# Optimization experiments

Hardware: AMD Instinct MI355X
Metric: run time of the kernel (lower is better)

Reference implementation:

```python
import jax, jax.numpy as jnp
import numpy as np

B, S, D = 1, 2048, 1024
H, HD = 16, 64            # heads, head_dim = D // H
TEN, ED, K = 32, 128, 8   # experts, expert_dim, top_k
DS = 2048                 # shared expert dim
THETA = 10000.0
EPS = 1e-6
RSF = 2.5                 # routed_scaling_factor


def setup_inputs() -> dict:
    key = jax.random.key(0)
    ks = jax.random.split(key, 12)
    s = 0.02
    return {
        "x_input": jax.random.normal(ks[0], (B, S, D), jnp.float32),
        "indices": jax.random.randint(ks[1], (B * S, K), 0, TEN, dtype=jnp.int32),
        "values": jax.random.normal(ks[2], (B * S, K), jnp.float32),
        "w_attn": jax.random.normal(ks[3], (D, 3 * D), jnp.float32) * s,
        "w_attn_o": jax.random.normal(ks[4], (D, D), jnp.float32) * s,
        "attn_norm_w": jnp.ones((D,), jnp.float32),
        "ffn_norm_w": jnp.ones((D,), jnp.float32),
        "ffn_experts": jax.random.normal(ks[5], (3, TEN, D, ED), jnp.float32) * s,
        "keys_w": jax.random.normal(ks[6], (D, TEN), jnp.float32) * s,
        "w_up": jax.random.normal(ks[7], (D, 2 * DS), jnp.float32) * s,
        "w_down": jax.random.normal(ks[8], (DS, D), jnp.float32) * s,
    }


def rmsnorm(x, w):
    return x * jax.lax.rsqrt(jnp.mean(x * x, -1, keepdims=True) + EPS) * w


def l2norm(x):
    # F.normalize(x, dim=-1, eps=EPS)
    n = jnp.sqrt(jnp.sum(x * x, -1, keepdims=True))
    return x / jnp.maximum(n, EPS)


def rope(x):
    # x: [B, H, S, HD]
    t = jnp.arange(x.shape[2], dtype=jnp.float32)
    inv = (1.0 / THETA) ** (jnp.arange(0, HD, 2, dtype=jnp.float32) / HD)
    f = jnp.outer(t, inv)[None, None]  # [1,1,S,HD//2]
    cos, sin = jnp.cos(f), jnp.sin(f)
    x1, x2 = jnp.split(x, 2, -1)
    return jnp.concatenate([x1 * cos + x2 * sin, -x1 * sin + x2 * cos], -1)


def reference(x_input, indices, values, w_attn, w_attn_o, attn_norm_w,
              ffn_norm_w, ffn_experts, keys_w, w_up, w_down):
    # ---- attention block ----
    x = rmsnorm(x_input, attn_norm_w)
    qkv = x @ w_attn  # [B,S,3D]
    xq, xk, xv = jnp.split(qkv, 3, -1)
    to_heads = lambda t: t.reshape(B, S, H, HD).transpose(0, 2, 1, 3)  # b h s a
    xq, xk, xv = to_heads(xq), to_heads(xk), to_heads(xv)
    xq, xk = l2norm(xq), l2norm(xk)  # qk_norm
    xq, xk = rope(xq), rope(xk)
    scores = jnp.einsum('bhqd,bhkd->bhqk', xq, xk) / jnp.sqrt(jnp.float32(HD))
    causal = jnp.tril(jnp.ones((S, S), bool))
    scores = jnp.where(causal, scores, jnp.finfo(scores.dtype).min)
    probs = jax.nn.softmax(scores, -1)
    x_attn = jnp.einsum('bhqk,bhkd->bhqd', probs, xv)
    x_attn = x_attn.transpose(0, 2, 1, 3).reshape(B, S, D)
    x_attn_o = x_attn @ w_attn_o
    x_ffn_input = x_attn_o + x_input

    # ---- router ----
    x_ffn = rmsnorm(x_ffn_input, ffn_norm_w)
    xf = x_ffn.reshape(B * S, D)
    logits = xf @ keys_w  # [T, TEN]
    token_values = jnp.take_along_axis(logits, indices, -1)  # [T, K]
    gates = jax.nn.sigmoid(values + token_values) * RSF

    # ---- grouped-GEMM expert dispatch (dense equivalent: combine is linear in score) ----
    T = B * S
    w_route = jnp.zeros((T, TEN), xf.dtype).at[jnp.arange(T)[:, None], indices].add(gates)
    g = jnp.einsum('td,edh->teh', xf, ffn_experts[0])
    u = jnp.einsum('td,edh->teh', xf, ffn_experts[1])
    h = jax.nn.silu(g) * u * w_route[:, :, None]
    y = jnp.einsum('teh,edh->td', h, ffn_experts[2]).reshape(B, S, D)

    # ---- shared expert (SwiGLU FFN) ----
    x1, x2 = jnp.split(x_ffn @ w_up, 2, -1)
    y_shared = (jax.nn.silu(x1) * x2) @ w_down
    y = y + y_shared
    return y + x_ffn_input
```

## Files before the change

### kernel.cpp

```cpp
#include <hip/hip_runtime.h>
#include <math.h>

#define TOKENS 2048
#define DIM 1024
#define NHEADS 16
#define HEADDIM 64
#define NEXP 32
#define EDIM 128
#define TOPK 8
#define DSHARED 2048
#define RSF_ 2.5f
#define EPS_ 1e-6f

using bf8  = __attribute__((ext_vector_type(8))) short;
using f32x4 = __attribute__((ext_vector_type(4))) float;

__device__ __forceinline__ short f2bf(float f) {
    unsigned u = __float_as_uint(f);
    unsigned r = (u + 0x7fffu + ((u >> 16) & 1u)) >> 16;
    return (short)r;
}
__device__ __forceinline__ float bf2f(short s) {
    return __uint_as_float(((unsigned)(unsigned short)s) << 16);
}

__device__ __forceinline__ void async16(const short* g, const short* l) {
    __builtin_amdgcn_global_load_lds(
        (const __attribute__((address_space(1))) void*)(unsigned long long)g,
        (__attribute__((address_space(3))) void*)(unsigned)(unsigned long long)l,
        16, 0, 0);
}

__global__ __launch_bounds__(256) void rmsnorm_kernel(const float* __restrict__ x,
                                                      const float* __restrict__ w,
                                                      short* __restrict__ out) {
    int row = blockIdx.x;
    const float* xr = x + (long long)row * DIM;
    int t = threadIdx.x;
    float4 xv = ((const float4*)xr)[t];
    float ss = xv.x*xv.x + xv.y*xv.y + xv.z*xv.z + xv.w*xv.w;
    #pragma unroll
    for (int off = 32; off; off >>= 1) ss += __shfl_down(ss, off);
    __shared__ float warps[4];
    if ((t & 63) == 0) warps[t >> 6] = ss;
    __syncthreads();
    float tot = warps[0] + warps[1] + warps[2] + warps[3];
    float scale = rsqrtf(tot / (float)DIM + EPS_);
    float4 wv = ((const float4*)w)[t];
    short4 o;
    o.x = f2bf(xv.x * scale * wv.x);
    o.y = f2bf(xv.y * scale * wv.y);
    o.z = f2bf(xv.z * scale * wv.z);
    o.w = f2bf(xv.w * scale * wv.w);
    ((short4*)(out + (long long)row * DIM))[t] = o;
}

__global__ __launch_bounds__(256) void tconv(const float* __restrict__ in, long long sin,
                                             short* __restrict__ out, long long sout,
                                             int K, int N) {
    in  += (long long)blockIdx.z * sin;
    out += (long long)blockIdx.z * sout;
    __shared__ float t[32][33];
    int n0 = blockIdx.x * 32, k0 = blockIdx.y * 32;
    int tx = threadIdx.x & 31, ty = threadIdx.x >> 5;
    #pragma unroll
    for (int r = ty; r < 32; r += 8)
        t[r][tx] = in[(long long)(k0 + r) * N + n0 + tx];
    __syncthreads();
    #pragma unroll
    for (int r = ty; r < 32; r += 8)
        out[(long long)(n0 + r) * K + k0 + tx] = f2bf(t[tx][r]);
}

__global__ void w2conv(const float* __restrict__ in, short* __restrict__ out) {
    long long i = (long long)blockIdx.x * 256 + threadIdx.x;
    int e = (int)(i >> 17);
    int d = (int)(i >> 7) & 1023;
    int h = (int)(i & 127);
    out[(long long)d * (NEXP * EDIM) + e * EDIM + h] = f2bf(in[i]);
}

template<int MODE>
__global__ __launch_bounds__(256) void gemm_bf16(const short* __restrict__ A, int lda, long long sA,
                                                 const short* __restrict__ Bt, int ldb, long long sBt,
                                                 void* __restrict__ Cv, int ldc, long long sC,
                                                 int M, int N, int K) {
    int koff = 0, Ksub = K;
    if (MODE >= 3) {
        Ksub = K / gridDim.z;
        koff = blockIdx.z * Ksub;
    } else {
        A  += (long long)blockIdx.z * sA;
        Bt += (long long)blockIdx.z * sBt;
    }
    float* Cf = (float*)Cv;
    short* Cs = (short*)Cv;
    Cf += (long long)blockIdx.z * sC;
    Cs += (long long)blockIdx.z * sC;
    const int m0 = blockIdx.y * 128, n0 = blockIdx.x * 128;
    __shared__ short As[128 * 64];
    __shared__ short Bs[128 * 64];
    const int tid = threadIdx.x, lane = tid & 63, w = tid >> 6;
    const int wm = (w >> 1) * 64, wn = (w & 1) * 64;
    const int drow = lane >> 3;
    const int dcol = ((lane & 7) ^ drow) * 8;
    const short* ag = A + (long long)(m0 + w * 32 + drow) * lda + koff + dcol;
    const short* bg = Bt + (long long)(n0 + w * 32 + drow) * ldb + koff + dcol;
    const short* lA = As + w * 32 * 64;
    const short* lB = Bs + w * 32 * 64;
    f32x4 acc[4][4];
    #pragma unroll
    for (int i = 0; i < 4; ++i)
        #pragma unroll
        for (int j = 0; j < 4; ++j) { f32x4 z = {0.f, 0.f, 0.f, 0.f}; acc[i][j] = z; }
    const int ra = lane & 15, quad = lane >> 4;
    const int fs0 = ((quad + 0) ^ (ra & 7)) * 8;
    const int fs1 = ((quad + 4) ^ (ra & 7)) * 8;
    for (int k0 = 0; k0 < Ksub; k0 += 64) {
        #pragma unroll
        for (int c = 0; c < 4; ++c) {
            async16(ag + (long long)(c * 8) * lda + k0, lA + c * 512);
            async16(bg + (long long)(c * 8) * ldb + k0, lB + c * 512);
        }
        __syncthreads();
        #pragma unroll
        for (int h = 0; h < 2; ++h) {
            const int fs = h ? fs1 : fs0;
            bf8 af[4], bfv[4];
            #pragma unroll
            for (int i = 0; i < 4; ++i) af[i]  = *(const bf8*)(As + (wm + i * 16 + ra) * 64 + fs);
            #pragma unroll
            for (int j = 0; j < 4; ++j) bfv[j] = *(const bf8*)(Bs + (wn + j * 16 + ra) * 64 + fs);
            #pragma unroll
            for (int i = 0; i < 4; ++i)
                #pragma unroll
                for (int j = 0; j < 4; ++j)
                    acc[i][j] = __builtin_amdgcn_mfma_f32_16x16x32_bf16(af[i], bfv[j], acc[i][j], 0, 0, 0);
        }
        __syncthreads();
    }
    const int cr = quad * 4, cc = ra;
    #pragma unroll
    for (int i = 0; i < 4; ++i) {
        #pragma unroll
        for (int r = 0; r < 4; ++r) {
            int row = m0 + wm + i * 16 + cr + r;
            long long base = (long long)row * ldc + n0 + wn + cc;
            #pragma unroll
            for (int j = 0; j < 4; ++j) {
                float v = acc[i][j][r];
                if (MODE == 0 || MODE == 3) Cf[base + j * 16] = v;
                if (MODE == 2) Cs[base + j * 16] = f2bf(v);
                if (MODE == 4) Cf[base + j * 16] = Cf[base + j * 16] + v;
            }
        }
    }
}

__global__ void combine4(const float* __restrict__ slices, const float* __restrict__ add,
                         float* __restrict__ dst) {
    long long i = (long long)blockIdx.x * 256 + threadIdx.x;
    const long long S4 = (long long)TOKENS * DIM / 4;
    float4 s = ((const float4*)add)[i];
    #pragma unroll
    for (int c = 0; c < 4; ++c) {
        float4 p = ((const float4*)slices)[c * S4 + i];
        s.x += p.x; s.y += p.y; s.z += p.z; s.w += p.w;
    }
    ((float4*)dst)[i] = s;
}

__global__ __launch_bounds__(256) void qkv_post(const short* __restrict__ qkv,
                                                short* __restrict__ q,
                                                short* __restrict__ k) {
    int lane = threadIdx.x & 63;
    int sh = blockIdx.x * 4 + (threadIdx.x >> 6);
    int s = sh >> 4;
    int h = sh & 15;
    const short* base = qkv + (long long)s * 3 * DIM;
    float qv = bf2f(base[h * HEADDIM + lane]);
    float kv = bf2f(base[DIM + h * HEADDIM + lane]);
    float qs = qv * qv, ks = kv * kv;
    #pragma unroll
    for (int off = 32; off; off >>= 1) {
        qs += __shfl_xor(qs, off);
        ks += __shfl_xor(ks, off);
    }
    qv /= fmaxf(sqrtf(qs), EPS_);
    kv /= fmaxf(sqrtf(ks), EPS_);
    int i = lane & 31;
    float f = (float)s * powf(10000.0f, -(float)i / 32.0f);
    float c = cosf(f), sn = sinf(f);
    float qo = __shfl_xor(qv, 32);
    float ko = __shfl_xor(kv, 32);
    float sgn = (lane < 32) ? sn : -sn;
    float qr = qv * c + qo * sgn;
    float kr = kv * c + ko * sgn;
    long long o = ((long long)h * TOKENS + s) * HEADDIM + lane;
    q[o] = f2bf(qr);
    k[o] = f2bf(kr);
}

__global__ __launch_bounds__(256) void vtrans(const short* __restrict__ qkv,
                                              short* __restrict__ vt) {
    int h = blockIdx.z;
    int s0 = blockIdx.x * 32, d0 = blockIdx.y * 32;
    __shared__ short t[32][34];
    int tx = threadIdx.x & 31, ty = threadIdx.x >> 5;
    #pragma unroll
    for (int r = ty; r < 32; r += 8)
        t[r][tx] = qkv[(long long)(s0 + r) * (3 * DIM) + 2 * DIM + h * HEADDIM + d0 + tx];
    __syncthreads();
    #pragma unroll
    for (int r = ty; r < 32; r += 8)
        vt[((long long)h * HEADDIM + d0 + r) * TOKENS + s0 + tx] = t[tx][r];
}

#define PLD 68
__global__ __launch_bounds__(256) void attn_kernel(const short* __restrict__ q,
                                                   const short* __restrict__ k,
                                                   const short* __restrict__ vt,
                                                   float* __restrict__ Oacc,
                                                   float* __restrict__ lacc) {
    const int w = threadIdx.x >> 6, lane = threadIdx.x & 63;
    const int col = lane & 15, quad = lane >> 4;
    const int head = blockIdx.x / 80;
    const int t = blockIdx.x % 80;
    int qb, ch;
    if (t < 8)       { qb = t;                ch = 0; }
    else if (t < 24) { qb = 8 + (t - 8) / 2;  ch = (t - 8) % 2; }
    else if (t < 48) { qb = 16 + (t - 24) / 3; ch = (t - 24) % 3; }
    else             { qb = 24 + (t - 48) / 4; ch = (t - 48) % 4; }
    const int nch = qb / 8 + 1;
    const int ntk = qb + 1;
    const int per = (ntk + nch - 1) / nch;
    const int t0 = ch * per;
    const int t1 = (t0 + per < ntk) ? t0 + per : ntk;
    const int qbase = qb * 64 + w * 16;
    __shared__ short Ks[64 * 64];
    __shared__ short Vs[64 * 64];
    __shared__ short Ps[4 * 16 * PLD];
    short* Pw = Ps + w * 16 * PLD;
    const short* kh = k + (long long)head * TOKENS * HEADDIM;
    const short* vh = vt + (long long)head * HEADDIM * TOKENS;
    const int r8 = lane >> 3;
    const int sw = ((lane & 7) ^ r8) * 8;
    bf8 qf[2];
    #pragma unroll
    for (int ks = 0; ks < 2; ++ks)
        qf[ks] = *(const bf8*)(q + ((long long)head * TOKENS + qbase + col) * HEADDIM + ks * 32 + quad * 8);
    const int fo0 = (((0 * 4) + quad) ^ (col & 7)) * 8;
    const int fo1 = (((1 * 4) + quad) ^ (col & 7)) * 8;
    f32x4 o_[4];
    float l_[4];
    #pragma unroll
    for (int n = 0; n < 4; ++n) { f32x4 z = {0.f, 0.f, 0.f, 0.f}; o_[n] = z; }
    #pragma unroll
    for (int r = 0; r < 4; ++r) l_[r] = 0.f;
    for (int kt = t0; kt < t1; ++kt) {
        const int j0 = kt * 64;
        #pragma unroll
        for (int c = 0; c < 2; ++c) {
            int row = w * 16 + c * 8 + r8;
            async16(kh + (long long)(j0 + row) * HEADDIM + sw, Ks + (w * 16 + c * 8) * 64 + lane * 8);
            async16(vh + (long long)row * TOKENS + j0 + sw, Vs + (w * 16 + c * 8) * 64 + lane * 8);
        }
        __syncthreads();
        f32x4 sacc[4];
        #pragma unroll
        for (int n = 0; n < 4; ++n) { f32x4 z = {0.f, 0.f, 0.f, 0.f}; sacc[n] = z; }
        #pragma unroll
        for (int ks = 0; ks < 2; ++ks) {
            const int fo = ks ? fo1 : fo0;
            #pragma unroll
            for (int nt = 0; nt < 4; ++nt) {
                bf8 kf = *(const bf8*)(Ks + (nt * 16 + col) * 64 + fo);
                sacc[nt] = __builtin_amdgcn_mfma_f32_16x16x32_bf16(qf[ks], kf, sacc[nt], 0, 0, 0);
            }
        }
        const bool diag = (j0 + 64 > qbase);
        #pragma unroll
        for (int nt = 0; nt < 4; ++nt)
            #pragma unroll
            for (int r = 0; r < 4; ++r) {
                float p = __expf(sacc[nt][r] * 0.125f);
                if (diag && (j0 + nt * 16 + col > qbase + quad * 4 + r)) p = 0.f;
                l_[r] += p;
                Pw[(quad * 4 + r) * PLD + nt * 16 + col] = f2bf(p);
            }
        #pragma unroll
        for (int ks = 0; ks < 2; ++ks) {
            bf8 pf = *(const bf8*)(Pw + col * PLD + ks * 32 + quad * 8);
            const int fo = ks ? fo1 : fo0;
            #pragma unroll
            for (int nt = 0; nt < 4; ++nt) {
                bf8 vf = *(const bf8*)(Vs + (nt * 16 + col) * 64 + fo);
                o_[nt] = __builtin_amdgcn_mfma_f32_16x16x32_bf16(pf, vf, o_[nt], 0, 0, 0);
            }
        }
        __syncthreads();
    }
    float* Oc = Oacc + (long long)ch * (TOKENS * DIM);
    #pragma unroll
    for (int r = 0; r < 4; ++r) {
        int row = qbase + quad * 4 + r;
        float* op = Oc + (long long)row * DIM + head * HEADDIM;
        #pragma unroll
        for (int nt = 0; nt < 4; ++nt)
            op[nt * 16 + col] = o_[nt][r];
        float l = l_[r];
        #pragma unroll
        for (int off = 1; off < 16; off <<= 1) l += __shfl_xor(l, off);
        if (col == 0) lacc[ch * (TOKENS * NHEADS) + row * NHEADS + head] = l;
    }
}

__global__ void attn_norm(const float* __restrict__ Oacc, const float* __restrict__ lacc,
                          short* __restrict__ xo) {
    long long i = (long long)blockIdx.x * 256 + threadIdx.x;
    int row = (int)(i >> 10), col = (int)(i & 1023);
    int nch = (row >> 9) + 1;
    int head = col >> 6;
    float so = 0.f, sl = 0.f;
    for (int c = 0; c < nch; ++c) {
        so += Oacc[(long long)c * (TOKENS * DIM) + i];
        sl += lacc[c * (TOKENS * NHEADS) + row * NHEADS + head];
    }
    xo[i] = f2bf(so / sl);
}

__global__ __launch_bounds__(256) void router_kernel(const short* __restrict__ xf,
                                                     const float* __restrict__ keys_w,
                                                     const int* __restrict__ idx,
                                                     const float* __restrict__ vals,
                                                     float* __restrict__ w_route) {
    int t = blockIdx.x;
    int tid = threadIdx.x;
    int e = tid & 31, c = tid >> 5;
    const short* xr = xf + (long long)t * DIM;
    float p = 0.f;
    for (int j = 0; j < 128; ++j)
        p += bf2f(xr[c * 128 + j]) * keys_w[(c * 128 + j) * NEXP + e];
    __shared__ float part[8][32];
    part[c][e] = p;
    __syncthreads();
    if (tid < NEXP) {
        float lg = 0.f;
        #pragma unroll
        for (int cc = 0; cc < 8; ++cc) lg += part[cc][tid];
        part[0][tid] = lg;
    }
    __syncthreads();
    __shared__ float gate_s[TOPK];
    __shared__ int idx_s[TOPK];
    if (tid < TOPK) {
        int ii = idx[t * TOPK + tid];
        float g = vals[t * TOPK + tid] + part[0][ii];
        gate_s[tid] = (1.0f / (1.0f + __expf(-g))) * RSF_;
        idx_s[tid] = ii;
    }
    __syncthreads();
    if (tid < NEXP) {
        float wr = 0.f;
        #pragma unroll
        for (int kk = 0; kk < TOPK; ++kk)
            if (idx_s[kk] == tid) wr += gate_s[kk];
        w_route[(long long)t * NEXP + tid] = wr;
    }
}

__global__ void moe_act_kernel(const short* __restrict__ gu, const float* __restrict__ w_route,
                               short* __restrict__ hb) {
    long long i = (long long)blockIdx.x * 256 + threadIdx.x;
    int t = (int)(i >> 12);
    int e = (int)(i >> 7) & 31;
    int j = (int)(i & 127);
    float gv = bf2f(gu[(long long)t * (NEXP * 256) + e * 256 + j]);
    float uv = bf2f(gu[(long long)t * (NEXP * 256) + e * 256 + 128 + j]);
    float w = w_route[t * NEXP + e];
    float si = gv / (1.0f + __expf(-gv));
    hb[i] = f2bf(si * uv * w);
}

__global__ void swiglu_kernel(const short* __restrict__ up, short* __restrict__ hs) {
    long long i = (long long)blockIdx.x * 256 + threadIdx.x;
    int t = (int)(i >> 11), j = (int)(i & 2047);
    float x1 = bf2f(up[(long long)t * (2 * DSHARED) + j]);
    float x2 = bf2f(up[(long long)t * (2 * DSHARED) + DSHARED + j]);
    hs[i] = f2bf(x1 / (1.0f + __expf(-x1)) * x2);
}

extern "C" void kernel_launch(void* const* d_in, const int* in_sizes, int n_in,
                              void* d_out, int out_size, void* d_ws, size_t ws_size,
                              hipStream_t stream) {
    (void)in_sizes; (void)n_in; (void)out_size; (void)ws_size;
    const float* x_input     = (const float*)d_in[0];
    const int*   indices     = (const int*)d_in[1];
    const float* values      = (const float*)d_in[2];
    const float* w_attn      = (const float*)d_in[3];
    const float* w_attn_o    = (const float*)d_in[4];
    const float* attn_norm_w = (const float*)d_in[5];
    const float* ffn_norm_w  = (const float*)d_in[6];
    const float* ffn_experts = (const float*)d_in[7];
    const float* keys_w      = (const float*)d_in[8];
    const float* w_up        = (const float*)d_in[9];
    const float* w_down      = (const float*)d_in[10];
    float* out = (float*)d_out;
    float* ws  = (float*)d_ws;

    const long long M1 = 1024 * 1024;
    const long long SLICE = (long long)TOKENS * DIM;
    float* xffn    = ws + 0 * M1;
    short* xa_bf   = (short*)(ws + 4 * M1);
    short* xf_bf   = (short*)(ws + 4 * M1 + M1 / 2);
    short* xattn_bf= (short*)(ws + 5 * M1);
    float* w_route = ws + 5 * M1 + M1 / 2;
    short* qkv_bf  = (short*)(ws + 6 * M1);
    float* Oacc    = ws + 6 * M1;
    float* lacc    = ws + 14 * M1;
    short* qh_bf   = (short*)(ws + 15 * M1);
    short* kh_bf   = (short*)(ws + 15 * M1 + M1 / 2);
    short* vt_bf   = (short*)(ws + 16 * M1);
    short* wattn_t = (short*)(ws + 17 * M1);
    short* wattno_t= (short*)(ws + 18 * M1 + M1 / 2);
    float* oslice  = ws + 6 * M1;
    short* wgu     = (short*)(ws + 6 * M1);
    short* gu_bf   = (short*)(ws + 10 * M1);
    short* h_bf    = (short*)(ws + 18 * M1);
    short* w2t     = (short*)(ws + 22 * M1);
    float* yslice  = ws + 6 * M1;
    short* wupt    = (short*)(ws + 14 * M1);
    short* up_bf   = (short*)(ws + 16 * M1);
    short* hs_bf   = (short*)(ws + 20 * M1);
    short* wdownt  = (short*)(ws + 22 * M1);

    const long long EXP_STRIDE = (long long)NEXP * DIM * EDIM;

    tconv<<<dim3(3072 / 32, DIM / 32, 1), 256, 0, stream>>>(w_attn, 0, wattn_t, 0, DIM, 3 * DIM);
    rmsnorm_kernel<<<TOKENS, 256, 0, stream>>>(x_input, attn_norm_w, xa_bf);
    gemm_bf16<2><<<dim3(3072 / 128, TOKENS / 128, 1), 256, 0, stream>>>(
        xa_bf, DIM, 0, wattn_t, DIM, 0, qkv_bf, 3 * DIM, 0, TOKENS, 3 * DIM, DIM);
    qkv_post<<<(TOKENS * NHEADS) / 4, 256, 0, stream>>>(qkv_bf, qh_bf, kh_bf);
    vtrans<<<dim3(TOKENS / 32, HEADDIM / 32, NHEADS), 256, 0, stream>>>(qkv_bf, vt_bf);
    attn_kernel<<<NHEADS * 80, 256, 0, stream>>>(qh_bf, kh_bf, vt_bf, Oacc, lacc);
    attn_norm<<<(TOKENS * DIM) / 256, 256, 0, stream>>>(Oacc, lacc, xattn_bf);
    tconv<<<dim3(DIM / 32, DIM / 32, 1), 256, 0, stream>>>(w_attn_o, 0, wattno_t, 0, DIM, DIM);
    gemm_bf16<3><<<dim3(DIM / 128, TOKENS / 128, 4), 256, 0, stream>>>(
        xattn_bf, DIM, 0, wattno_t, DIM, 0, oslice, DIM, SLICE, TOKENS, DIM, DIM);
    combine4<<<(TOKENS * DIM) / 1024, 256, 0, stream>>>(oslice, x_input, xffn);

    rmsnorm_kernel<<<TOKENS, 256, 0, stream>>>(xffn, ffn_norm_w, xf_bf);
    router_kernel<<<TOKENS, 256, 0, stream>>>(xf_bf, keys_w, indices, values, w_route);
    tconv<<<dim3(EDIM / 32, DIM / 32, NEXP), 256, 0, stream>>>(
        ffn_experts, (long long)DIM * EDIM, wgu, 256 * 1024, DIM, EDIM);
    tconv<<<dim3(EDIM / 32, DIM / 32, NEXP), 256, 0, stream>>>(
        ffn_experts + EXP_STRIDE, (long long)DIM * EDIM, wgu + 128 * 1024, 256 * 1024, DIM, EDIM);
    gemm_bf16<2><<<dim3(2, TOKENS / 128, NEXP), 256, 0, stream>>>(
        xf_bf, DIM, 0, wgu, DIM, 256 * 1024, gu_bf, NEXP * 256, 256, TOKENS, 256, DIM);
    moe_act_kernel<<<(TOKENS * NEXP * EDIM) / 256, 256, 0, stream>>>(gu_bf, w_route, h_bf);
    w2conv<<<(NEXP * DIM * EDIM) / 256, 256, 0, stream>>>(ffn_experts + 2 * EXP_STRIDE, w2t);
    gemm_bf16<3><<<dim3(DIM / 128, TOKENS / 128, 4), 256, 0, stream>>>(
        h_bf, NEXP * EDIM, 0, w2t, NEXP * EDIM, 0, yslice, DIM, SLICE, TOKENS, DIM, NEXP * EDIM);

    tconv<<<dim3((2 * DSHARED) / 32, DIM / 32, 1), 256, 0, stream>>>(w_up, 0, wupt, 0, DIM, 2 * DSHARED);
    gemm_bf16<2><<<dim3((2 * DSHARED) / 128, TOKENS / 128, 1), 256, 0, stream>>>(
        xf_bf, DIM, 0, wupt, DIM, 0, up_bf, 2 * DSHARED, 0, TOKENS, 2 * DSHARED, DIM);
    swiglu_kernel<<<(TOKENS * DSHARED) / 256, 256, 0, stream>>>(up_bf, hs_bf);
    tconv<<<dim3(DIM / 32, DSHARED / 32, 1), 256, 0, stream>>>(w_down, 0, wdownt, 0, DSHARED, DIM);
    gemm_bf16<4><<<dim3(DIM / 128, TOKENS / 128, 4), 256, 0, stream>>>(
        hs_bf, DSHARED, 0, wdownt, DSHARED, 0, yslice, DIM, SLICE, TOKENS, DIM, DSHARED);

    combine4<<<(TOKENS * DIM) / 1024, 256, 0, stream>>>(yslice, xffn, out);
}
```

Measured before the change: 444.6 us.

## Fuse SwiGLU activations into gate/up GEMM epilogues and fuse residual with RMSNorm

Adds a gemm_act kernel that computes the gate and up projections together, using interleaved weight rows produced by new guconv/upconv transposes, and applies SiLU(g)*u (optionally scaled by the routing weight) in the epilogue. This removes the separate moe_act and swiglu passes and the bf16 intermediate gate/up tensors. It also merges combine4 with the second rmsnorm into one combine_rms kernel, and reorganizes workspace offsets. The risk is that the new GEMM uses 64-row tiles without double buffering, which may be less efficient than the existing gemm_bf16.

```diff
diff --git a/kernel.cpp b/kernel.cpp
--- a/kernel.cpp
+++ b/kernel.cpp
@@ -78,6 +78,45 @@
     int d = (int)(i >> 7) & 1023;
     int h = (int)(i & 127);
     out[(long long)d * (NEXP * EDIM) + e * EDIM + h] = f2bf(in[i]);
+}
+
+__global__ __launch_bounds__(256) void guconv(const float* __restrict__ ex,
+                                              short* __restrict__ wgu) {
+    int z = blockIdx.z;
+    int e = z & 31, hf = z >> 5;
+    const float* in = ex + (long long)hf * (NEXP * DIM * EDIM) + (long long)e * (DIM * EDIM);
+    short* outp = wgu + (long long)e * (256 * 1024);
+    __shared__ float t[32][33];
+    int n0 = blockIdx.x * 32, k0 = blockIdx.y * 32;
+    int tx = threadIdx.x & 31, ty = threadIdx.x >> 5;
+    #pragma unroll
+    for (int r = ty; r < 32; r += 8)
+        t[r][tx] = in[(long long)(k0 + r) * EDIM + n0 + tx];
+    __syncthreads();
+    #pragma unroll
+    for (int r = ty; r < 32; r += 8) {
+        int c = n0 + r;
+        int rr = ((c >> 4) << 5) + hf * 16 + (c & 15);
+        outp[(long long)rr * 1024 + k0 + tx] = f2bf(t[tx][r]);
+    }
+}
+
+__global__ __launch_bounds__(256) void upconv(const float* __restrict__ in,
+                                              short* __restrict__ outp) {
+    __shared__ float t[32][33];
+    int n0 = blockIdx.x * 32, k0 = blockIdx.y * 32;
+    int tx = threadIdx.x & 31, ty = threadIdx.x >> 5;
+    #pragma unroll
+    for (int r = ty; r < 32; r += 8)
+        t[r][tx] = in[(long long)(k0 + r) * (2 * DSHARED) + n0 + tx];
+    __syncthreads();
+    #pragma unroll
+    for (int r = ty; r < 32; r += 8) {
+        int n = n0 + r;
+        int hf = n >> 11, c2 = n & 2047;
+        int rr = ((c2 >> 7) << 8) + (((c2 & 127) >> 4) << 5) + hf * 16 + (c2 & 15);
+        outp[(long long)rr * 1024 + k0 + tx] = f2bf(t[tx][r]);
+    }
 }
 
 template<int MODE>
@@ -149,12 +188,75 @@
             #pragma unroll
             for (int j = 0; j < 4; ++j) {
                 float v = acc[i][j][r];
-                if (MODE == 0 || MODE == 3) Cf[base + j * 16] = v;
                 if (MODE == 2) Cs[base + j * 16] = f2bf(v);
+                if (MODE == 3) Cf[base + j * 16] = v;
                 if (MODE == 4) Cf[base + j * 16] = Cf[base + j * 16] + v;
             }
         }
     }
+}
+
+template<bool SCALED>
+__global__ __launch_bounds__(256) void gemm_act(const short* __restrict__ A, int lda,
+                                                const short* __restrict__ Bt, long long sBt,
+                                                short* __restrict__ Ct, int ldct,
+                                                const float* __restrict__ wr) {
+    const short* Bp = Bt + (long long)blockIdx.z * sBt + (long long)blockIdx.x * (256 * 1024);
+    const int cb = (blockIdx.z * gridDim.x + blockIdx.x) * 128;
+    const int m0 = blockIdx.y * 64;
+    __shared__ short As[64 * 64];
+    __shared__ short Bs[256 * 64];
+    const int tid = threadIdx.x, lane = tid & 63, w = tid >> 6;
+    const int wm = (w >> 1) * 32, wn = (w & 1) * 128;
+    const int drow = lane >> 3;
+    const int dcol = ((lane & 7) ^ drow) * 8;
+    const short* ag = A + (long long)(m0 + w * 16 + drow) * lda + dcol;
+    const short* bg = Bp + (long long)(w * 64 + drow) * 1024 + dcol;
+    const short* lA = As + w * 16 * 64;
+    const short* lB = Bs + w * 64 * 64;
+    f32x4 acc[2][8];
+    #pragma unroll
+    for (int i = 0; i < 2; ++i)
+        #pragma unroll
+        for (int j = 0; j < 8; ++j) { f32x4 z = {0.f, 0.f, 0.f, 0.f}; acc[i][j] = z; }
+    const int ra = lane & 15, quad = lane >> 4;
+    const int fs0 = ((quad + 0) ^ (ra & 7)) * 8;
+    const int fs1 = ((quad + 4) ^ (ra & 7)) * 8;
+    for (int k0 = 0; k0 < 1024; k0 += 64) {
+        async16(ag + k0, lA);
+        async16(ag + (long long)8 * lda + k0, lA + 512);
+        #pragma unroll
+        for (int c = 0; c < 8; ++c)
+            async16(bg + (long long)(c * 8) * 1024 + k0, lB + c * 512);
+        __syncthreads();
+        #pragma unroll
+        for (int h = 0; h < 2; ++h) {
+            const int fs = h ? fs1 : fs0;
+            bf8 af0 = *(const bf8*)(As + (wm + ra) * 64 + fs);
+            bf8 af1 = *(const bf8*)(As + (wm + 16 + ra) * 64 + fs);
+            #pragma unroll
+            for (int j = 0; j < 8; ++j) {
+                bf8 bv = *(const bf8*)(Bs + (wn + j * 16 + ra) * 64 + fs);
+                acc[0][j] = __builtin_amdgcn_mfma_f32_16x16x32_bf16(af0, bv, acc[0][j], 0, 0, 0);
+                acc[1][j] = __builtin_amdgcn_mfma_f32_16x16x32_bf16(af1, bv, acc[1][j], 0, 0, 0);
+            }
+        }
+        __syncthreads();
+    }
+    #pragma unroll
+    for (int i = 0; i < 2; ++i)
+        #pragma unroll
+        for (int r = 0; r < 4; ++r) {
+            int token = m0 + wm + i * 16 + quad * 4 + r;
+            float scale = SCALED ? wr[token * NEXP + blockIdx.z] : 1.0f;
+            #pragma unroll
+            for (int jp = 0; jp < 4; ++jp) {
+                float g = acc[i][2 * jp][r];
+                float u = acc[i][2 * jp + 1][r];
+                float v = g / (1.0f + __expf(-g)) * u * scale;
+                Ct[(long long)token * ldct + cb + wn / 2 + jp * 16 + ra] = f2bf(v);
+            }
+        }
 }
 
 __global__ void combine4(const float* __restrict__ slices, const float* __restrict__ add,
@@ -168,6 +270,38 @@
         s.x += p.x; s.y += p.y; s.z += p.z; s.w += p.w;
     }
     ((float4*)dst)[i] = s;
+}
+
+__global__ __launch_bounds__(256) void combine_rms(const float* __restrict__ slices,
+                                                   const float* __restrict__ add,
+                                                   const float* __restrict__ w,
+                                                   float* __restrict__ xffn,
+                                                   short* __restrict__ xf) {
+    int row = blockIdx.x, t = threadIdx.x;
+    long long i = (long long)row * 256 + t;
+    const long long S4 = (long long)TOKENS * DIM / 4;
+    float4 s = ((const float4*)add)[i];
+    #pragma unroll
+    for (int c = 0; c < 4; ++c) {
+        float4 p = ((const float4*)slices)[c * S4 + i];
+        s.x += p.x; s.y += p.y; s.z += p.z; s.w += p.w;
+    }
+    ((float4*)xffn)[i] = s;
+    float ss = s.x*s.x + s.y*s.y + s.z*s.z + s.w*s.w;
+    #pragma unroll
+    for (int off = 32; off; off >>= 1) ss += __shfl_down(ss, off);
+    __shared__ float warps[4];
+    if ((t & 63) == 0) warps[t >> 6] = ss;
+    __syncthreads();
+    float tot = warps[0] + warps[1] + warps[2] + warps[3];
+    float scale = rsqrtf(tot / (float)DIM + EPS_);
+    float4 wv = ((const float4*)w)[t];
+    short4 o;
+    o.x = f2bf(s.x * scale * wv.x);
+    o.y = f2bf(s.y * scale * wv.y);
+    o.z = f2bf(s.z * scale * wv.z);
+    o.w = f2bf(s.w * scale * wv.w);
+    ((short4*)(xf + (long long)row * DIM))[t] = o;
 }
 
 __global__ __launch_bounds__(256) void qkv_post(const short* __restrict__ qkv,
@@ -369,27 +503,6 @@
     }
 }
 
-__global__ void moe_act_kernel(const short* __restrict__ gu, const float* __restrict__ w_route,
-                               short* __restrict__ hb) {
-    long long i = (long long)blockIdx.x * 256 + threadIdx.x;
-    int t = (int)(i >> 12);
-    int e = (int)(i >> 7) & 31;
-    int j = (int)(i & 127);
-    float gv = bf2f(gu[(long long)t * (NEXP * 256) + e * 256 + j]);
-    float uv = bf2f(gu[(long long)t * (NEXP * 256) + e * 256 + 128 + j]);
-    float w = w_route[t * NEXP + e];
-    float si = gv / (1.0f + __expf(-gv));
-    hb[i] = f2bf(si * uv * w);
-}
-
-__global__ void swiglu_kernel(const short* __restrict__ up, short* __restrict__ hs) {
-    long long i = (long long)blockIdx.x * 256 + threadIdx.x;
-    int t = (int)(i >> 11), j = (int)(i & 2047);
-    float x1 = bf2f(up[(long long)t * (2 * DSHARED) + j]);
-    float x2 = bf2f(up[(long long)t * (2 * DSHARED) + DSHARED + j]);
-    hs[i] = f2bf(x1 / (1.0f + __expf(-x1)) * x2);
-}
-
 extern "C" void kernel_launch(void* const* d_in, const int* in_sizes, int n_in,
                               void* d_out, int out_size, void* d_ws, size_t ws_size,
                               hipStream_t stream) {
@@ -415,7 +528,6 @@
     short* xf_bf   = (short*)(ws + 4 * M1 + M1 / 2);
     short* xattn_bf= (short*)(ws + 5 * M1);
     float* w_route = ws + 5 * M1 + M1 / 2;
-    short* qkv_bf  = (short*)(ws + 6 * M1);
     float* Oacc    = ws + 6 * M1;
     float* lacc    = ws + 14 * M1;
     short* qh_bf   = (short*)(ws + 15 * M1);
@@ -423,18 +535,15 @@
     short* vt_bf   = (short*)(ws + 16 * M1);
     short* wattn_t = (short*)(ws + 17 * M1);
     short* wattno_t= (short*)(ws + 18 * M1 + M1 / 2);
+    short* qkv_bf  = (short*)(ws + 21 * M1);
     float* oslice  = ws + 6 * M1;
     short* wgu     = (short*)(ws + 6 * M1);
-    short* gu_bf   = (short*)(ws + 10 * M1);
-    short* h_bf    = (short*)(ws + 18 * M1);
-    short* w2t     = (short*)(ws + 22 * M1);
-    float* yslice  = ws + 6 * M1;
-    short* wupt    = (short*)(ws + 14 * M1);
-    short* up_bf   = (short*)(ws + 16 * M1);
-    short* hs_bf   = (short*)(ws + 20 * M1);
-    short* wdownt  = (short*)(ws + 22 * M1);
-
-    const long long EXP_STRIDE = (long long)NEXP * DIM * EDIM;
+    short* h_bf    = (short*)(ws + 10 * M1);
+    short* w2t     = (short*)(ws + 14 * M1);
+    float* yslice  = ws + 16 * M1;
+    short* wupt    = (short*)(ws + 6 * M1);
+    short* hs_bf   = (short*)(ws + 8 * M1);
+    short* wdownt  = (short*)(ws + 10 * M1);
 
     tconv<<<dim3(3072 / 32, DIM / 32, 1), 256, 0, stream>>>(w_attn, 0, wattn_t, 0, DIM, 3 * DIM);
     rmsnorm_kernel<<<TOKENS, 256, 0, stream>>>(x_input, attn_norm_w, xa_bf);
@@ -447,25 +556,20 @@
     tconv<<<dim3(DIM / 32, DIM / 32, 1), 256, 0, stream>>>(w_attn_o, 0, wattno_t, 0, DIM, DIM);
     gemm_bf16<3><<<dim3(DIM / 128, TOKENS / 128, 4), 256, 0, stream>>>(
         xattn_bf, DIM, 0, wattno_t, DIM, 0, oslice, DIM, SLICE, TOKENS, DIM, DIM);
-    combine4<<<(TOKENS * DIM) / 1024, 256, 0, stream>>>(oslice, x_input, xffn);
-
-    rmsnorm_kernel<<<TOKENS, 256, 0, stream>>>(xffn, ffn_norm_w, xf_bf);
+    combine_rms<<<TOKENS, 256, 0, stream>>>(oslice, x_input, ffn_norm_w, xffn, xf_bf);
+
     router_kernel<<<TOKENS, 256, 0, stream>>>(xf_bf, keys_w, indices, values, w_route);
-    tconv<<<dim3(EDIM / 32, DIM / 32, NEXP), 256, 0, stream>>>(
-        ffn_experts, (long long)DIM * EDIM, wgu, 256 * 1024, DIM, EDIM);
-    tconv<<<dim3(EDIM / 32, DIM / 32, NEXP), 256, 0, stream>>>(
-        ffn_experts + EXP_STRIDE, (long long)DIM * EDIM, wgu + 128 * 1024, 256 * 1024, DIM, EDIM);
-    gemm_bf16<2><<<dim3(2, TOKENS / 128, NEXP), 256, 0, stream>>>(
-        xf_bf, DIM, 0, wgu, DIM, 256 * 1024, gu_bf, NEXP * 256, 256, TOKENS, 256, DIM);
-    moe_act_kernel<<<(TOKENS * NEXP * EDIM) / 256, 256, 0, stream>>>(gu_bf, w_route, h_bf);
-    w2conv<<<(NEXP * DIM * EDIM) / 256, 256, 0, stream>>>(ffn_experts + 2 * EXP_STRIDE, w2t);
+    guconv<<<dim3(EDIM / 32, DIM / 32, 2 * NEXP), 256, 0, stream>>>(ffn_experts, wgu);
+    gemm_act<true><<<dim3(1, TOKENS / 64, NEXP), 256, 0, stream>>>(
+        xf_bf, DIM, wgu, 256 * 1024, h_bf, NEXP * EDIM, w_route);
+    w2conv<<<(NEXP * DIM * EDIM) / 256, 256, 0, stream>>>(
+        ffn_experts + 2LL * NEXP * DIM * EDIM, w2t);
     gemm_bf16<3><<<dim3(DIM / 128, TOKENS / 128, 4), 256, 0, stream>>>(
         h_bf, NEXP * EDIM, 0, w2t, NEXP * EDIM, 0, yslice, DIM, SLICE, TOKENS, DIM, NEXP * EDIM);
 
-    tconv<<<dim3((2 * DSHARED) / 32, DIM / 32, 1), 256, 0, stream>>>(w_up, 0, wupt, 0, DIM, 2 * DSHARED);
-    gemm_bf16<2><<<dim3((2 * DSHARED) / 128, TOKENS / 128, 1), 256, 0, stream>>>(
-        xf_bf, DIM, 0, wupt, DIM, 0, up_bf, 2 * DSHARED, 0, TOKENS, 2 * DSHARED, DIM);
-    swiglu_kernel<<<(TOKENS * DSHARED) / 256, 256, 0, stream>>>(up_bf, hs_bf);
+    upconv<<<dim3((2 * DSHARED) / 32, DIM / 32, 1), 256, 0, stream>>>(w_up, wupt);
+    gemm_act<false><<<dim3((2 * DSHARED) / 256, TOKENS / 64, 1), 256, 0, stream>>>(
+        xf_bf, DIM, wupt, 0, hs_bf, DSHARED, nullptr);
     tconv<<<dim3(DIM / 32, DSHARED / 32, 1), 256, 0, stream>>>(w_down, 0, wdownt, 0, DSHARED, DIM);
     gemm_bf16<4><<<dim3(DIM / 128, TOKENS / 128, 4), 256, 0, stream>>>(
         hs_bf, DSHARED, 0, wdownt, DSHARED, 0, yslice, DIM, SLICE, TOKENS, DIM, DSHARED);
```

Result: faster. 420.7 us (-5.4%).
